# Optimization experiments

Hardware: AMD Instinct MI355X
Metric: run time of the kernel (lower is better)

Reference implementation:

```python
import jax, jax.numpy as jnp
import numpy as np

N, H, B = 8192, 32, 256
AVG_DEG = 32.0


def setup_inputs() -> dict:
    key = jax.random.key(0)
    ks = jax.random.split(key, 16)
    z = jax.random.normal(ks[0], (N, H), jnp.float32)
    # binary adjacency with ~AVG_DEG neighbors per node; S = row-normalized A
    A = (jax.random.uniform(ks[1], (N, N)) < (AVG_DEG / N)).astype(jnp.float32)
    deg = A.sum(1, keepdims=True)
    S = jnp.where(deg > 0, A / jnp.maximum(deg, 1.0), 0.0)
    u_idx = jax.random.randint(ks[2], (B,), 0, N, dtype=jnp.int32)
    v_idx = jax.random.randint(ks[3], (B,), 0, N, dtype=jnp.int32)
    k = jax.random.randint(ks[4], (B,), 0, 2, dtype=jnp.int32)
    time_delta = jax.random.uniform(ks[5], (B, 2, 4), jnp.float32)

    def lin(kk, o, i):  # xavier-ish init
        return jax.random.normal(kk, (o, i), jnp.float32) * (1.0 / np.sqrt(i))

    return dict(
        z=z, A=A, S=S, u_idx=u_idx, v_idx=v_idx, k=k, time_delta=time_delta,
        W_h_w=lin(ks[6], H, H), W_h_b=jnp.zeros(H, jnp.float32),
        W_struct_w=lin(ks[7], H, H), W_struct_b=jnp.zeros(H, jnp.float32),
        W_rec_w=lin(ks[8], H, H), W_rec_b=jnp.zeros(H, jnp.float32),
        W_t_w=lin(ks[9], H, 4), W_t_b=jnp.zeros(H, jnp.float32),
        om0_w=lin(ks[10], 1, 2 * H), om0_b=jnp.zeros(1, jnp.float32),
        om1_w=lin(ks[11], 1, 2 * H), om1_b=jnp.zeros(1, jnp.float32),
        psi=0.5 * jnp.ones(2, jnp.float32),
    )


def reference(z, A, S, u_idx, v_idx, k, time_delta,
              W_h_w, W_h_b, W_struct_w, W_struct_b,
              W_rec_w, W_rec_b, W_t_w, W_t_b,
              om0_w, om0_b, om1_w, om1_b, psi):
    kpos = k > 0  # [B]

    # ---- intensity_rate_lambda (non-bilinear g_fn, edge_type=None) ----
    zu, zv = z[u_idx], z[v_idx]                      # [B,H]
    cat_uv = jnp.concatenate([zu, zv], axis=1)       # [B,2H]
    cat_vu = jnp.concatenate([zv, zu], axis=1)

    def g_fn(zc):  # selects omega[0] for k<=0, omega[1] for k>0
        g0 = (zc @ om0_w.T + om0_b)[:, 0]
        g1 = (zc @ om1_w.T + om1_b)[:, 0]
        return jnp.where(kpos, g1, g0)

    g = 0.5 * (g_fn(cat_uv) + g_fn(cat_vu))          # [B]
    psi_k = psi[kpos.astype(jnp.int32)]
    g_psi = jnp.clip(g / (psi_k + 1e-7), -75.0, 75.0)
    Lambda = psi_k * (jnp.log1p(jnp.exp(-g_psi)) + g_psi)

    # ---- update_node_embed: S-weighted neighbor aggregation + RNN-style update ----
    h_all = z @ W_h_w.T + W_h_b                      # W_h(z) for all nodes [N,H]
    targets = jnp.stack([u_idx, v_idx], axis=1)      # nodes being updated [B,2]
    partners = jnp.stack([v_idx, u_idx], axis=1)     # struct comes from partner

    mask = A[partners] > 0                           # [B,2,N] neighbor mask
    q = jnp.exp(S[partners]) * mask                  # attention over neighbors
    q = q / (q.sum(-1, keepdims=True) + 1e-7)
    sig = jax.nn.sigmoid(q[..., None] * h_all[None, None])   # [B,2,N,H]
    h_struct = jnp.where(mask[..., None], sig, -jnp.inf).max(axis=2)  # [B,2,H]
    has_nb = mask.any(-1, keepdims=True)
    h_struct = jnp.where(has_nb, h_struct, 0.0)

    h1 = h_struct @ W_struct_w.T + W_struct_b        # [B,2,H]
    z_new = jax.nn.sigmoid(h1 + z[targets] @ W_rec_w.T + W_rec_b
                           + time_delta @ W_t_w.T + W_t_b)  # [B,2,H]
    return Lambda, z_new
```

## Files before the change

kernel.cpp:

```cpp
#include <hip/hip_runtime.h>
#include <hip/hip_bf16.h>
#include <math.h>

#define H 32
#define NT 256
#define MAXNBR 512
#define CHUNK 64
#define TP 33

__global__ __launch_bounds__(NT) void fused_kernel(
    const float* __restrict__ S,
    const float* __restrict__ z,
    const int* __restrict__ u_idx, const int* __restrict__ v_idx,
    const int* __restrict__ k,
    const float* __restrict__ time_delta,
    const float* __restrict__ W_h_w, const float* __restrict__ W_h_b,
    const float* __restrict__ W_struct_w, const float* __restrict__ W_struct_b,
    const float* __restrict__ W_rec_w, const float* __restrict__ W_rec_b,
    const float* __restrict__ W_t_w, const float* __restrict__ W_t_b,
    const float* __restrict__ om0_w, const float* __restrict__ om0_b,
    const float* __restrict__ om1_w, const float* __restrict__ om1_b,
    const float* __restrict__ psi,
    float* __restrict__ out_lambda,
    float* __restrict__ out_znew,
    int N)
{
    int pair = blockIdx.x;
    int b = pair >> 1;
    int j = pair & 1;
    int u = u_idx[b], v = v_idx[b];
    int target  = (j == 0) ? u : v;
    int partner = (j == 0) ? v : u;

    __shared__ float WhT[H * TP];
    __shared__ float WsT[H * TP];
    __shared__ float WrT[H * TP];
    __shared__ float WtT[4 * TP];
    __shared__ float Bsh[H];
    __shared__ float s_bias[H];
    __shared__ float s_zt[H];
    __shared__ float s_td[4];
    __shared__ int   s_cnt;
    __shared__ int   s_nbr[MAXNBR];
    __shared__ float zsh[CHUNK][H];
    __shared__ float s_max[8][H];
    __shared__ float s_hstruct[H];

    int tid = threadIdx.x;
    if (tid == 0) s_cnt = 0;

    float4 wh4 = ((const float4*)W_h_w)[tid];
    float4 ws4 = ((const float4*)W_struct_w)[tid];
    float4 wr4 = ((const float4*)W_rec_w)[tid];
    float  wt1 = (tid < 4 * H) ? W_t_w[tid] : 0.f;
    float  bh  = (tid < H) ? W_h_b[tid] : 0.f;
    float  bsm = (tid < H) ? (W_struct_b[tid] + W_rec_b[tid] + W_t_b[tid]) : 0.f;
    float  ztv = (tid < H) ? z[(size_t)target * H + tid] : 0.f;
    float  tdv = (tid < 4) ? time_delta[(size_t)pair * 4 + tid] : 0.f;

    const float4* Srow4 = (const float4*)(S + (size_t)partner * N);
    int n4 = N >> 2;
    bool fast = (n4 == 2048);
    float4 sv[8];
    if (fast) {
#pragma unroll
        for (int r = 0; r < 8; r++) sv[r] = Srow4[tid + r * NT];
    }

    if (j == 0 && tid >= NT - 32) {
        int l = tid - (NT - 32);
        bool kpos = k[b] > 0;
        const float* om_w = kpos ? om1_w : om0_w;
        float g = (om_w[l] + om_w[l + H]) *
                  (z[(size_t)u * H + l] + z[(size_t)v * H + l]);
#pragma unroll
        for (int off = 16; off > 0; off >>= 1) g += __shfl_xor(g, off, 32);
        if (l == 0) {
            float om_bias = kpos ? om1_b[0] : om0_b[0];
            g = 0.5f * g + om_bias;
            float psi_k = psi[kpos ? 1 : 0];
            float gp = g / (psi_k + 1e-7f);
            gp = fminf(fmaxf(gp, -75.f), 75.f);
            out_lambda[b] = psi_k * (log1pf(expf(-gp)) + gp);
        }
    }

    {
        int i0 = 4 * tid;
        int hh = i0 >> 5;
        const float* whp = (const float*)&wh4;
        const float* wsp = (const float*)&ws4;
        const float* wrp = (const float*)&wr4;
#pragma unroll
        for (int c = 0; c < 4; c++) {
            int jj = (i0 + c) & 31;
            WhT[jj * TP + hh] = whp[c];
            WsT[jj * TP + hh] = wsp[c];
            WrT[jj * TP + hh] = wrp[c];
        }
        if (tid < 4 * H) WtT[(tid & 3) * TP + (tid >> 2)] = wt1;
        if (tid < H) { Bsh[tid] = bh; s_bias[tid] = bsm; s_zt[tid] = ztv; }
        if (tid < 4) s_td[tid] = tdv;
    }
    __syncthreads();

    if (fast) {
#pragma unroll
        for (int r = 0; r < 8; r++) {
            float4 s4 = sv[r];
            float m4 = fmaxf(fmaxf(s4.x, s4.y), fmaxf(s4.z, s4.w));
            if (m4 > 0.f) {
                const float* sp = (const float*)&s4;
#pragma unroll
                for (int c = 0; c < 4; c++) {
                    if (sp[c] > 0.f) {
                        int pos = atomicAdd(&s_cnt, 1);
                        if (pos < MAXNBR) s_nbr[pos] = (tid + r * NT) * 4 + c;
                    }
                }
            }
        }
    } else {
        for (int it = tid; it < n4; it += NT) {
            float4 s4 = Srow4[it];
            const float* sp = (const float*)&s4;
#pragma unroll
            for (int c = 0; c < 4; c++) {
                if (sp[c] > 0.f) {
                    int pos = atomicAdd(&s_cnt, 1);
                    if (pos < MAXNBR) s_nbr[pos] = it * 4 + c;
                }
            }
        }
    }
    __syncthreads();
    int cnt = s_cnt;
    int cnt_l = (cnt > MAXNBR) ? MAXNBR : cnt;
    float e_s = expf(1.f / (float)((cnt > 0) ? cnt : 1));
    float q = e_s / ((float)cnt * e_s + 1e-7f);

    int grp = tid >> 5;
    int h   = tid & 31;
    float mmax = -INFINITY;
    for (int base = 0; base < cnt_l; base += CHUNK) {
        int m = min(CHUNK, cnt_l - base);
        for (int t = tid; t < m * 8; t += NT) {
            int i = t >> 3, c = t & 7;
            ((float4*)zsh[i])[c] =
                ((const float4*)(z + (size_t)s_nbr[base + i] * H))[c];
        }
        __syncthreads();
        for (int i = grp; i < m; i += 8) {
            float hv = Bsh[h];
#pragma unroll
            for (int jj = 0; jj < H; jj++)
                hv += WhT[jj * TP + h] * zsh[i][jj];
            mmax = fmaxf(mmax, hv);
        }
        __syncthreads();
    }
    s_max[grp][h] = mmax;
    __syncthreads();
    if (tid < H) {
        float mm = s_max[0][tid];
#pragma unroll
        for (int g = 1; g < 8; g++) mm = fmaxf(mm, s_max[g][tid]);
        s_hstruct[tid] = (cnt > 0) ? 1.f / (1.f + expf(-q * mm)) : 0.f;
    }
    __syncthreads();

    if (tid < H) {
        int hh = tid;
        float acc = s_bias[hh];
#pragma unroll
        for (int jj = 0; jj < H; jj++) {
            acc += WsT[jj * TP + hh] * s_hstruct[jj];
            acc += WrT[jj * TP + hh] * s_zt[jj];
        }
#pragma unroll
        for (int jj = 0; jj < 4; jj++) acc += WtT[jj * TP + hh] * s_td[jj];
        out_znew[(size_t)pair * H + hh] = 1.f / (1.f + expf(-acc));
    }
}

extern "C" void kernel_launch(void* const* d_in, const int* in_sizes, int n_in,
                              void* d_out, int out_size, void* d_ws, size_t ws_size,
                              hipStream_t stream) {
    const float* z          = (const float*)d_in[0];
    const float* S          = (const float*)d_in[2];
    const int*   u_idx      = (const int*)d_in[3];
    const int*   v_idx      = (const int*)d_in[4];
    const int*   k          = (const int*)d_in[5];
    const float* time_delta = (const float*)d_in[6];
    const float* W_h_w      = (const float*)d_in[7];
    const float* W_h_b      = (const float*)d_in[8];
    const float* W_struct_w = (const float*)d_in[9];
    const float* W_struct_b = (const float*)d_in[10];
    const float* W_rec_w    = (const float*)d_in[11];
    const float* W_rec_b    = (const float*)d_in[12];
    const float* W_t_w      = (const float*)d_in[13];
    const float* W_t_b      = (const float*)d_in[14];
    const float* om0_w      = (const float*)d_in[15];
    const float* om0_b      = (const float*)d_in[16];
    const float* om1_w      = (const float*)d_in[17];
    const float* om1_b      = (const float*)d_in[18];
    const float* psi        = (const float*)d_in[19];

    const int B = in_sizes[3];
    const int N = in_sizes[0] / H;
    float* out        = (float*)d_out;
    float* out_lambda = out;
    float* out_znew   = out + B;

    fused_kernel<<<B * 2, NT, 0, stream>>>(
        S, z, u_idx, v_idx, k, time_delta,
        W_h_w, W_h_b, W_struct_w, W_struct_b, W_rec_w, W_rec_b, W_t_w, W_t_b,
        om0_w, om0_b, om1_w, om1_b, psi,
        out_lambda, out_znew, N);
}
```

Measured before the change: 12.47 us.

## Merge both pair halves into one 512-thread block sharing weight staging

Each block now handles both update targets of a batch element, with two 256-thread halves scanning the two partner rows at once. The weight-transpose loads into shared memory are split between the halves, so each weight matrix is fetched once per block rather than per half-pair. The grid is halved, and the final struct vector is passed through a wavefront shuffle instead of shared memory, which drops one barrier. In exchange the blocks are larger, the halves are synchronised over the longer neighbour list, and the neighbour buffer shrinks to 256 entries.

```diff
diff --git a/kernel.cpp b/kernel.cpp
--- a/kernel.cpp
+++ b/kernel.cpp
@@ -3,8 +3,9 @@
 #include <math.h>
 
 #define H 32
-#define NT 256
-#define MAXNBR 512
+#define NT 512
+#define HT 256
+#define MAXNBR 256
 #define CHUNK 64
 #define TP 33
 
@@ -25,11 +26,12 @@
     float* __restrict__ out_znew,
     int N)
 {
-    int pair = blockIdx.x;
-    int b = pair >> 1;
-    int j = pair & 1;
+    int b = blockIdx.x;
+    int tid = threadIdx.x;
+    int j = tid >> 8;
+    int t = tid & (HT - 1);
+
     int u = u_idx[b], v = v_idx[b];
-    int target  = (j == 0) ? u : v;
     int partner = (j == 0) ? v : u;
 
     __shared__ float WhT[H * TP];
@@ -38,25 +40,31 @@
     __shared__ float WtT[4 * TP];
     __shared__ float Bsh[H];
     __shared__ float s_bias[H];
-    __shared__ float s_zt[H];
-    __shared__ float s_td[4];
-    __shared__ int   s_cnt;
-    __shared__ int   s_nbr[MAXNBR];
-    __shared__ float zsh[CHUNK][H];
-    __shared__ float s_max[8][H];
-    __shared__ float s_hstruct[H];
-
-    int tid = threadIdx.x;
-    if (tid == 0) s_cnt = 0;
-
-    float4 wh4 = ((const float4*)W_h_w)[tid];
-    float4 ws4 = ((const float4*)W_struct_w)[tid];
-    float4 wr4 = ((const float4*)W_rec_w)[tid];
-    float  wt1 = (tid < 4 * H) ? W_t_w[tid] : 0.f;
-    float  bh  = (tid < H) ? W_h_b[tid] : 0.f;
-    float  bsm = (tid < H) ? (W_struct_b[tid] + W_rec_b[tid] + W_t_b[tid]) : 0.f;
-    float  ztv = (tid < H) ? z[(size_t)target * H + tid] : 0.f;
-    float  tdv = (tid < 4) ? time_delta[(size_t)pair * 4 + tid] : 0.f;
+    __shared__ float s_zt[2][H];
+    __shared__ float s_td[2][4];
+    __shared__ int   s_cnt[2];
+    __shared__ int   s_nbr[2][MAXNBR];
+    __shared__ float zsh[2][CHUNK][H];
+    __shared__ float s_max[2][8][H];
+
+    if (t == 0) s_cnt[j] = 0;
+
+    float4 wA, wB;
+    float  wt1 = 0.f, bh = 0.f, bsm = 0.f, ztv = 0.f, tdv = 0.f;
+    if (j == 0) {
+        wA = ((const float4*)W_h_w)[t];
+        wB = ((const float4*)W_rec_w)[t];
+    } else {
+        wA = ((const float4*)W_struct_w)[t];
+        wB = make_float4(0.f, 0.f, 0.f, 0.f);
+        if (t < 4 * H) wt1 = W_t_w[t];
+        if (t >= 128 && t < 160) bh  = W_h_b[t - 128];
+        if (t >= 160 && t < 192) bsm = W_struct_b[t - 160] + W_rec_b[t - 160]
+                                     + W_t_b[t - 160];
+        if (t >= 192 && t < 224) ztv = z[(size_t)u * H + (t - 192)];
+        if (t >= 224)            ztv = z[(size_t)v * H + (t - 224)];
+    }
+    if (j == 0 && t < 8) tdv = time_delta[(size_t)b * 8 + t];
 
     const float4* Srow4 = (const float4*)(S + (size_t)partner * N);
     int n4 = N >> 2;
@@ -64,11 +72,11 @@
     float4 sv[8];
     if (fast) {
 #pragma unroll
-        for (int r = 0; r < 8; r++) sv[r] = Srow4[tid + r * NT];
-    }
-
-    if (j == 0 && tid >= NT - 32) {
-        int l = tid - (NT - 32);
+        for (int r = 0; r < 8; r++) sv[r] = Srow4[t + r * HT];
+    }
+
+    if (j == 0 && t >= HT - 32) {
+        int l = t - (HT - 32);
         bool kpos = k[b] > 0;
         const float* om_w = kpos ? om1_w : om0_w;
         float g = (om_w[l] + om_w[l + H]) *
@@ -86,21 +94,30 @@
     }
 
     {
-        int i0 = 4 * tid;
+        int i0 = 4 * t;
         int hh = i0 >> 5;
-        const float* whp = (const float*)&wh4;
-        const float* wsp = (const float*)&ws4;
-        const float* wrp = (const float*)&wr4;
-#pragma unroll
-        for (int c = 0; c < 4; c++) {
-            int jj = (i0 + c) & 31;
-            WhT[jj * TP + hh] = whp[c];
-            WsT[jj * TP + hh] = wsp[c];
-            WrT[jj * TP + hh] = wrp[c];
-        }
-        if (tid < 4 * H) WtT[(tid & 3) * TP + (tid >> 2)] = wt1;
-        if (tid < H) { Bsh[tid] = bh; s_bias[tid] = bsm; s_zt[tid] = ztv; }
-        if (tid < 4) s_td[tid] = tdv;
+        const float* ap = (const float*)&wA;
+        const float* bp = (const float*)&wB;
+        if (j == 0) {
+#pragma unroll
+            for (int c = 0; c < 4; c++) {
+                int jj = (i0 + c) & 31;
+                WhT[jj * TP + hh] = ap[c];
+                WrT[jj * TP + hh] = bp[c];
+            }
+            if (t < 8) s_td[t >> 2][t & 3] = tdv;
+        } else {
+#pragma unroll
+            for (int c = 0; c < 4; c++) {
+                int jj = (i0 + c) & 31;
+                WsT[jj * TP + hh] = ap[c];
+            }
+            if (t < 4 * H) WtT[(t & 3) * TP + (t >> 2)] = wt1;
+            if (t >= 128 && t < 160) Bsh[t - 128]    = bh;
+            if (t >= 160 && t < 192) s_bias[t - 160] = bsm;
+            if (t >= 192 && t < 224) s_zt[0][t - 192] = ztv;
+            if (t >= 224)            s_zt[1][t - 224] = ztv;
+        }
     }
     __syncthreads();
 
@@ -114,72 +131,78 @@
 #pragma unroll
                 for (int c = 0; c < 4; c++) {
                     if (sp[c] > 0.f) {
-                        int pos = atomicAdd(&s_cnt, 1);
-                        if (pos < MAXNBR) s_nbr[pos] = (tid + r * NT) * 4 + c;
+                        int pos = atomicAdd(&s_cnt[j], 1);
+                        if (pos < MAXNBR) s_nbr[j][pos] = (t + r * HT) * 4 + c;
                     }
                 }
             }
         }
     } else {
-        for (int it = tid; it < n4; it += NT) {
+        for (int it = t; it < n4; it += HT) {
             float4 s4 = Srow4[it];
             const float* sp = (const float*)&s4;
 #pragma unroll
             for (int c = 0; c < 4; c++) {
                 if (sp[c] > 0.f) {
-                    int pos = atomicAdd(&s_cnt, 1);
-                    if (pos < MAXNBR) s_nbr[pos] = it * 4 + c;
+                    int pos = atomicAdd(&s_cnt[j], 1);
+                    if (pos < MAXNBR) s_nbr[j][pos] = it * 4 + c;
                 }
             }
         }
     }
     __syncthreads();
-    int cnt = s_cnt;
+
+    int cnt  = s_cnt[j];
     int cnt_l = (cnt > MAXNBR) ? MAXNBR : cnt;
+    int cnt0 = s_cnt[0] > MAXNBR ? MAXNBR : s_cnt[0];
+    int cnt1 = s_cnt[1] > MAXNBR ? MAXNBR : s_cnt[1];
+    int nch = ((cnt0 > cnt1 ? cnt0 : cnt1) + CHUNK - 1) / CHUNK;
     float e_s = expf(1.f / (float)((cnt > 0) ? cnt : 1));
     float q = e_s / ((float)cnt * e_s + 1e-7f);
 
-    int grp = tid >> 5;
-    int h   = tid & 31;
+    int grp = t >> 5;
+    int h   = t & 31;
     float mmax = -INFINITY;
-    for (int base = 0; base < cnt_l; base += CHUNK) {
-        int m = min(CHUNK, cnt_l - base);
-        for (int t = tid; t < m * 8; t += NT) {
-            int i = t >> 3, c = t & 7;
-            ((float4*)zsh[i])[c] =
-                ((const float4*)(z + (size_t)s_nbr[base + i] * H))[c];
+    for (int kc = 0; kc < nch; kc++) {
+        int base = kc * CHUNK;
+        int m = cnt_l - base;
+        if (m > CHUNK) m = CHUNK;
+        if (m > 0) {
+            for (int tt = t; tt < m * 8; tt += HT) {
+                int i = tt >> 3, c = tt & 7;
+                ((float4*)zsh[j][i])[c] =
+                    ((const float4*)(z + (size_t)s_nbr[j][base + i] * H))[c];
+            }
         }
         __syncthreads();
-        for (int i = grp; i < m; i += 8) {
-            float hv = Bsh[h];
-#pragma unroll
-            for (int jj = 0; jj < H; jj++)
-                hv += WhT[jj * TP + h] * zsh[i][jj];
-            mmax = fmaxf(mmax, hv);
-        }
-        __syncthreads();
-    }
-    s_max[grp][h] = mmax;
+        if (m > 0) {
+            for (int i = grp; i < m; i += 8) {
+                float hv = Bsh[h];
+#pragma unroll
+                for (int jj = 0; jj < H; jj++)
+                    hv += WhT[jj * TP + h] * zsh[j][i][jj];
+                mmax = fmaxf(mmax, hv);
+            }
+        }
+        if (kc + 1 < nch) __syncthreads();
+    }
+    s_max[j][grp][h] = mmax;
     __syncthreads();
-    if (tid < H) {
-        float mm = s_max[0][tid];
-#pragma unroll
-        for (int g = 1; g < 8; g++) mm = fmaxf(mm, s_max[g][tid]);
-        s_hstruct[tid] = (cnt > 0) ? 1.f / (1.f + expf(-q * mm)) : 0.f;
-    }
-    __syncthreads();
-
-    if (tid < H) {
-        int hh = tid;
-        float acc = s_bias[hh];
+
+    if (t < H) {
+        float mm = s_max[j][0][t];
+#pragma unroll
+        for (int g = 1; g < 8; g++) mm = fmaxf(mm, s_max[j][g][t]);
+        float hst = (cnt > 0) ? 1.f / (1.f + expf(-q * mm)) : 0.f;
+        float acc = s_bias[t];
 #pragma unroll
         for (int jj = 0; jj < H; jj++) {
-            acc += WsT[jj * TP + hh] * s_hstruct[jj];
-            acc += WrT[jj * TP + hh] * s_zt[jj];
-        }
-#pragma unroll
-        for (int jj = 0; jj < 4; jj++) acc += WtT[jj * TP + hh] * s_td[jj];
-        out_znew[(size_t)pair * H + hh] = 1.f / (1.f + expf(-acc));
+            acc += WsT[jj * TP + t] * __shfl(hst, jj, 32);
+            acc += WrT[jj * TP + t] * s_zt[j][jj];
+        }
+#pragma unroll
+        for (int jj = 0; jj < 4; jj++) acc += WtT[jj * TP + t] * s_td[j][jj];
+        out_znew[((size_t)b * 2 + j) * H + t] = 1.f / (1.f + expf(-acc));
     }
 }
 
@@ -212,7 +235,7 @@
     float* out_lambda = out;
     float* out_znew   = out + B;
 
-    fused_kernel<<<B * 2, NT, 0, stream>>>(
+    fused_kernel<<<B, NT, 0, stream>>>(
         S, z, u_idx, v_idx, k, time_delta,
         W_h_w, W_h_b, W_struct_w, W_struct_b, W_rec_w, W_rec_b, W_t_w, W_t_b,
         om0_w, om0_b, om1_w, om1_b, psi,
```

Measured after the change: 12.44 us, median of 2. No clear change (-0.2%).
